# Optimization experiments

Measured on AMD Instinct MI355X. Metric: run time of the kernel, lower is better.

## Reference

```python
import jax, jax.numpy as jnp
import numpy as np

B, L, C, K = 8, 4096, 256, 3
PAD = 1  # (K-1)//2, required so offset/mask conv preserves length L


def conv1d(x, w, b, padding):
    # x: (B, C, L), w: (O, C, K), b: (O,)
    y = jax.lax.conv_general_dilated(
        x, w, window_strides=(1,), padding=[(padding, padding)],
        dimension_numbers=('NCH', 'OIH', 'NCH'))
    return y + b[None, :, None]


def setup_inputs() -> dict:
    key = jax.random.key(0)
    ks = jax.random.split(key, 5)
    fan = 1.0 / np.sqrt(C * K)
    return {
        'x': jax.random.normal(ks[0], (B, L, C), dtype=jnp.float32),
        'w_off': jax.random.uniform(ks[1], (K, C, K), jnp.float32, -fan, fan),
        'b_off': jax.random.uniform(ks[2], (K,), jnp.float32, -fan, fan),
        'w_mask': jax.random.uniform(ks[3], (K, C, K), jnp.float32, -fan, fan),
        'b_mask': jax.random.uniform(ks[4], (K,), jnp.float32, -fan, fan),
    }


def reference(x, w_off, b_off, w_mask, b_mask):
    b, l, c = x.shape
    xt = jnp.transpose(x, (0, 2, 1))                      # (B, C, L)
    offset = conv1d(xt, w_off, b_off, PAD)                # (B, K, L)
    mask = jax.nn.sigmoid(conv1d(xt, w_mask, b_mask, PAD))  # (B, K, L)

    # pos = l + offset, clamped; offset is shared across channels.
    i = jnp.arange(l, dtype=x.dtype)[None, None, :]       # (1, 1, L)
    pos = jnp.clip(i + offset, 0.0, l - 1)                # (B, K, L)
    fl = jnp.floor(pos).astype(jnp.int32)                 # (B, K, L)
    ce = jnp.minimum(fl + 1, l - 1)
    alpha = pos - fl.astype(x.dtype)                      # (B, K, L)

    # gather per batch: (C, L)[:, (K, L)] -> (C, K, L)
    gather = jax.vmap(lambda xb, idx: xb[:, idx])
    x_floor = gather(xt, fl)                              # (B, C, K, L)
    x_ceil = gather(xt, ce)                               # (B, C, K, L)
    a = alpha[:, None, :, :]
    sampled = x_floor * (1.0 - a) + x_ceil * a            # (B, C, K, L)

    out = (sampled * mask[:, None, :, :]).sum(axis=2)     # (B, C, L)
    # Faithful to torch: output.view(B, L, out_channels) is a raw reshape
    # of the contiguous (B, C, L) buffer, NOT a transpose.
    return out.reshape(b, l, c)
```

## Files before the change

kernel.cpp:

```cpp
#include <hip/hip_runtime.h>
#include <math.h>

#define B_  8
#define L_  4096
#define C_  256
#define TL  32
#define NT  2

template<int CTRL, int RM>
__device__ __forceinline__ float dpp_add(float v) {
    int mv = __builtin_amdgcn_update_dpp(0, __float_as_int(v), CTRL, RM, 0xf, true);
    return v + __int_as_float(mv);
}
__device__ __forceinline__ float wave_sum_hi(float v) {
    v = dpp_add<0xB1, 0xf>(v);
    v = dpp_add<0x4E, 0xf>(v);
    v = dpp_add<0x141, 0xf>(v);
    v = dpp_add<0x140, 0xf>(v);
    v = dpp_add<0x142, 0xa>(v);
    v = dpp_add<0x143, 0xc>(v);
    return v;
}
__device__ __forceinline__ float bcast63(float v) {
    return __int_as_float(__builtin_amdgcn_readlane(__float_as_int(v), 63));
}

__global__ __launch_bounds__(512, 4)
void dconv1d_kernel(const float* __restrict__ x,
                    const float* __restrict__ w_off,
                    const float* __restrict__ b_off,
                    const float* __restrict__ w_mask,
                    const float* __restrict__ b_mask,
                    float* __restrict__ out) {
    __shared__ float s_tile[TL * C_];

    const int tid  = threadIdx.x;
    const int lane = tid & 63;
    const int wv   = tid >> 6;
    const int b    = blockIdx.y;
    const float* __restrict__ xb = x + (size_t)b * L_ * C_;

    const float bo0 = b_off[0],  bo1 = b_off[1],  bo2 = b_off[2];
    const float bm0 = b_mask[0], bm1 = b_mask[1], bm2 = b_mask[2];

    const int c4 = lane << 2;

    for (int t = 0; t < NT; ++t) {
        const int l0  = (blockIdx.x * NT + t) * TL;
        const int lb4 = l0 + wv * 4;

        float4 xrow[6];
        #pragma unroll
        for (int rr = 0; rr < 6; ++rr) {
            const int row = lb4 - 1 + rr;
            if (row >= 0 && row < L_)
                xrow[rr] = *reinterpret_cast<const float4*>(
                    xb + (size_t)row * C_ + c4);
            else
                xrow[rr] = make_float4(0.f, 0.f, 0.f, 0.f);
        }

        float sums[4][6];
        #pragma unroll
        for (int o = 0; o < 6; ++o) {
            const float* ws = (o < 3) ? (w_off + o * (C_ * 3))
                                      : (w_mask + (o - 3) * (C_ * 3));
            const float4* wp = reinterpret_cast<const float4*>(ws + lane * 12);
            const float4 w0 = wp[0], w1 = wp[1], w2 = wp[2];
            float acc[4] = {0.f, 0.f, 0.f, 0.f};
            #pragma unroll
            for (int rr = 0; rr < 6; ++rr) {
                #pragma unroll
                for (int tt = 0; tt < 3; ++tt) {
                    const int i = rr - tt;
                    if (i >= 0 && i < 4) {
                        const float wt0 = (tt==0)?w0.x:((tt==1)?w0.y:w0.z);
                        const float wt1 = (tt==0)?w0.w:((tt==1)?w1.x:w1.y);
                        const float wt2 = (tt==0)?w1.z:((tt==1)?w1.w:w2.x);
                        const float wt3 = (tt==0)?w2.y:((tt==1)?w2.z:w2.w);
                        acc[i] += xrow[rr].x * wt0 + xrow[rr].y * wt1
                                + xrow[rr].z * wt2 + xrow[rr].w * wt3;
                    }
                }
            }
            #pragma unroll
            for (int i = 0; i < 4; ++i)
                sums[i][o] = bcast63(wave_sum_hi(acc[i]));
        }

        #pragma unroll
        for (int i = 0; i < 4; ++i) {
            const int ll = wv * 4 + i;
            const int l  = l0 + ll;
            float4 v = make_float4(0.f, 0.f, 0.f, 0.f);
            #pragma unroll
            for (int k = 0; k < 3; ++k) {
                const float bo = (k == 0) ? bo0 : ((k == 1) ? bo1 : bo2);
                const float bm = (k == 0) ? bm0 : ((k == 1) ? bm1 : bm2);
                const float off = sums[i][k] + bo;
                const float pos = fminf(fmaxf((float)l + off, 0.0f), (float)(L_ - 1));
                const float flf = floorf(pos);
                const int   fl  = (int)flf;
                const int   ce  = min(fl + 1, L_ - 1);
                const float a   = pos - flf;
                const float m   = 1.0f / (1.0f + __expf(-(sums[i][k + 3] + bm)));
                const float wf  = m * (1.0f - a);
                const float wc  = m * a;
                const float4 xf = *reinterpret_cast<const float4*>(
                    xb + (size_t)fl * C_ + c4);
                const float4 xc = *reinterpret_cast<const float4*>(
                    xb + (size_t)ce * C_ + c4);
                v.x += wf * xf.x + wc * xc.x;
                v.y += wf * xf.y + wc * xc.y;
                v.z += wf * xf.z + wc * xc.z;
                v.w += wf * xf.w + wc * xc.w;
            }
            const int gr = lane ^ (ll & 15);
            *reinterpret_cast<float4*>(&s_tile[ll * C_ + (gr << 2)]) = v;
        }
        __syncthreads();

        {
            const int lw = tid & 31;
            const int q0 = tid >> 5;
            #pragma unroll
            for (int s = 0; s < 4; ++s) {
                const int q  = q0 + (s << 4);
                const int gr = q ^ (lw & 15);
                const float4 v = *reinterpret_cast<const float4*>(
                    &s_tile[lw * C_ + (gr << 2)]);
                const size_t ob = ((size_t)b * C_ + (q << 2)) * L_ + l0 + lw;
                out[ob]          = v.x;
                out[ob + L_]     = v.y;
                out[ob + 2 * L_] = v.z;
                out[ob + 3 * L_] = v.w;
            }
        }
        __syncthreads();
    }
}

extern "C" void kernel_launch(void* const* d_in, const int* in_sizes, int n_in,
                              void* d_out, int out_size, void* d_ws, size_t ws_size,
                              hipStream_t stream) {
    const float* x      = (const float*)d_in[0];
    const float* w_off  = (const float*)d_in[1];
    const float* b_off  = (const float*)d_in[2];
    const float* w_mask = (const float*)d_in[3];
    const float* b_mask = (const float*)d_in[4];
    float* out = (float*)d_out;

    dim3 grid(L_ / (TL * NT), B_);
    dconv1d_kernel<<<grid, 512, 0, stream>>>(x, w_off, b_off, w_mask, b_mask, out);
}
```

Measured before the change: 28.25 us.

## Stage x tile with halo in LDS and serve gathers from shared memory

Each block now loads a 40-row halo tile of x into LDS once. The conv reads and the deformable gather reads are served from LDS when the sampled positions fall within the tile, with a fallback to global memory otherwise. The block shrinks to 256 threads, each wave handles 8 positions, the NT loop goes away, and the grid doubles in x. The new layout uses more LDS per block (about 72KB), which lowers occupancy, and the tile must fill completely before any compute can start.

```diff
diff --git a/kernel.cpp b/kernel.cpp
--- a/kernel.cpp
+++ b/kernel.cpp
@@ -5,7 +5,8 @@
 #define L_  4096
 #define C_  256
 #define TL  32
-#define NT  2
+#define SROWS 40
+#define SBASE 4
 
 template<int CTRL, int RM>
 __device__ __forceinline__ float dpp_add(float v) {
@@ -25,18 +26,22 @@
     return __int_as_float(__builtin_amdgcn_readlane(__float_as_int(v), 63));
 }
 
-__global__ __launch_bounds__(512, 4)
+#define LDS_BARRIER() asm volatile("s_waitcnt lgkmcnt(0)\ns_barrier" ::: "memory")
+
+__global__ __launch_bounds__(256, 2)
 void dconv1d_kernel(const float* __restrict__ x,
                     const float* __restrict__ w_off,
                     const float* __restrict__ b_off,
                     const float* __restrict__ w_mask,
                     const float* __restrict__ b_mask,
                     float* __restrict__ out) {
+    __shared__ float s_x[SROWS * C_];
     __shared__ float s_tile[TL * C_];
 
     const int tid  = threadIdx.x;
     const int lane = tid & 63;
     const int wv   = tid >> 6;
+    const int l0   = blockIdx.x * TL;
     const int b    = blockIdx.y;
     const float* __restrict__ xb = x + (size_t)b * L_ * C_;
 
@@ -45,98 +50,104 @@
 
     const int c4 = lane << 2;
 
-    for (int t = 0; t < NT; ++t) {
-        const int l0  = (blockIdx.x * NT + t) * TL;
-        const int lb4 = l0 + wv * 4;
+    #pragma unroll
+    for (int j = 0; j < (SROWS * 64) / 256; ++j) {
+        const int idx  = j * 256 + tid;
+        const int r    = idx >> 6;
+        const int gq   = idx & 63;
+        const int grow = l0 - SBASE + r;
+        float4 v = make_float4(0.f, 0.f, 0.f, 0.f);
+        if (grow >= 0 && grow < L_)
+            v = *reinterpret_cast<const float4*>(xb + (size_t)grow * C_ + (gq << 2));
+        *reinterpret_cast<float4*>(&s_x[r * C_ + (gq << 2)]) = v;
+    }
+    LDS_BARRIER();
 
-        float4 xrow[6];
+    const int lw0 = wv * 8;
+    float sums[8][6];
+    #pragma unroll
+    for (int o = 0; o < 6; ++o) {
+        const float* ws = (o < 3) ? (w_off + o * (C_ * 3))
+                                  : (w_mask + (o - 3) * (C_ * 3));
+        const float4* wp = reinterpret_cast<const float4*>(ws + lane * 12);
+        const float4 w0 = wp[0], w1 = wp[1], w2 = wp[2];
+        float acc[8] = {0.f,0.f,0.f,0.f,0.f,0.f,0.f,0.f};
         #pragma unroll
-        for (int rr = 0; rr < 6; ++rr) {
-            const int row = lb4 - 1 + rr;
-            if (row >= 0 && row < L_)
-                xrow[rr] = *reinterpret_cast<const float4*>(
-                    xb + (size_t)row * C_ + c4);
-            else
-                xrow[rr] = make_float4(0.f, 0.f, 0.f, 0.f);
-        }
-
-        float sums[4][6];
-        #pragma unroll
-        for (int o = 0; o < 6; ++o) {
-            const float* ws = (o < 3) ? (w_off + o * (C_ * 3))
-                                      : (w_mask + (o - 3) * (C_ * 3));
-            const float4* wp = reinterpret_cast<const float4*>(ws + lane * 12);
-            const float4 w0 = wp[0], w1 = wp[1], w2 = wp[2];
-            float acc[4] = {0.f, 0.f, 0.f, 0.f};
+        for (int rr = 0; rr < 10; ++rr) {
+            const int srow = lw0 - 1 + rr + SBASE;
+            const float4 xv = *reinterpret_cast<const float4*>(
+                &s_x[srow * C_ + c4]);
             #pragma unroll
-            for (int rr = 0; rr < 6; ++rr) {
-                #pragma unroll
-                for (int tt = 0; tt < 3; ++tt) {
-                    const int i = rr - tt;
-                    if (i >= 0 && i < 4) {
-                        const float wt0 = (tt==0)?w0.x:((tt==1)?w0.y:w0.z);
-                        const float wt1 = (tt==0)?w0.w:((tt==1)?w1.x:w1.y);
-                        const float wt2 = (tt==0)?w1.z:((tt==1)?w1.w:w2.x);
-                        const float wt3 = (tt==0)?w2.y:((tt==1)?w2.z:w2.w);
-                        acc[i] += xrow[rr].x * wt0 + xrow[rr].y * wt1
-                                + xrow[rr].z * wt2 + xrow[rr].w * wt3;
-                    }
+            for (int tt = 0; tt < 3; ++tt) {
+                const int i = rr - tt;
+                if (i >= 0 && i < 8) {
+                    const float wt0 = (tt==0)?w0.x:((tt==1)?w0.y:w0.z);
+                    const float wt1 = (tt==0)?w0.w:((tt==1)?w1.x:w1.y);
+                    const float wt2 = (tt==0)?w1.z:((tt==1)?w1.w:w2.x);
+                    const float wt3 = (tt==0)?w2.y:((tt==1)?w2.z:w2.w);
+                    acc[i] += xv.x * wt0 + xv.y * wt1
+                            + xv.z * wt2 + xv.w * wt3;
                 }
             }
-            #pragma unroll
-            for (int i = 0; i < 4; ++i)
-                sums[i][o] = bcast63(wave_sum_hi(acc[i]));
         }
+        #pragma unroll
+        for (int i = 0; i < 8; ++i)
+            sums[i][o] = bcast63(wave_sum_hi(acc[i]));
+    }
 
+    #pragma unroll
+    for (int i = 0; i < 8; ++i) {
+        const int ll = lw0 + i;
+        const int l  = l0 + ll;
+        float4 v = make_float4(0.f, 0.f, 0.f, 0.f);
         #pragma unroll
-        for (int i = 0; i < 4; ++i) {
-            const int ll = wv * 4 + i;
-            const int l  = l0 + ll;
-            float4 v = make_float4(0.f, 0.f, 0.f, 0.f);
-            #pragma unroll
-            for (int k = 0; k < 3; ++k) {
-                const float bo = (k == 0) ? bo0 : ((k == 1) ? bo1 : bo2);
-                const float bm = (k == 0) ? bm0 : ((k == 1) ? bm1 : bm2);
-                const float off = sums[i][k] + bo;
-                const float pos = fminf(fmaxf((float)l + off, 0.0f), (float)(L_ - 1));
-                const float flf = floorf(pos);
-                const int   fl  = (int)flf;
-                const int   ce  = min(fl + 1, L_ - 1);
-                const float a   = pos - flf;
-                const float m   = 1.0f / (1.0f + __expf(-(sums[i][k + 3] + bm)));
-                const float wf  = m * (1.0f - a);
-                const float wc  = m * a;
-                const float4 xf = *reinterpret_cast<const float4*>(
-                    xb + (size_t)fl * C_ + c4);
-                const float4 xc = *reinterpret_cast<const float4*>(
-                    xb + (size_t)ce * C_ + c4);
-                v.x += wf * xf.x + wc * xc.x;
-                v.y += wf * xf.y + wc * xc.y;
-                v.z += wf * xf.z + wc * xc.z;
-                v.w += wf * xf.w + wc * xc.w;
+        for (int k = 0; k < 3; ++k) {
+            const float bo = (k == 0) ? bo0 : ((k == 1) ? bo1 : bo2);
+            const float bm = (k == 0) ? bm0 : ((k == 1) ? bm1 : bm2);
+            const float off = sums[i][k] + bo;
+            const float pos = fminf(fmaxf((float)l + off, 0.0f), (float)(L_ - 1));
+            const float flf = floorf(pos);
+            const int   fl  = (int)flf;
+            const int   ce  = min(fl + 1, L_ - 1);
+            const float a   = pos - flf;
+            const float m   = 1.0f / (1.0f + __expf(-(sums[i][k + 3] + bm)));
+            const float wf  = m * (1.0f - a);
+            const float wc  = m * a;
+            const int fr = fl - (l0 - SBASE);
+            const int cr = ce - (l0 - SBASE);
+            float4 xf, xc;
+            if (fr >= 0 && cr < SROWS) {
+                xf = *reinterpret_cast<const float4*>(&s_x[fr * C_ + c4]);
+                xc = *reinterpret_cast<const float4*>(&s_x[cr * C_ + c4]);
+            } else {
+                xf = *reinterpret_cast<const float4*>(xb + (size_t)fl * C_ + c4);
+                xc = *reinterpret_cast<const float4*>(xb + (size_t)ce * C_ + c4);
             }
-            const int gr = lane ^ (ll & 15);
-            *reinterpret_cast<float4*>(&s_tile[ll * C_ + (gr << 2)]) = v;
+            v.x += wf * xf.x + wc * xc.x;
+            v.y += wf * xf.y + wc * xc.y;
+            v.z += wf * xf.z + wc * xc.z;
+            v.w += wf * xf.w + wc * xc.w;
         }
-        __syncthreads();
+        const int gr = lane ^ (ll & 15);
+        *reinterpret_cast<float4*>(&s_tile[ll * C_ + (gr << 2)]) = v;
+    }
+    LDS_BARRIER();
 
-        {
-            const int lw = tid & 31;
-            const int q0 = tid >> 5;
-            #pragma unroll
-            for (int s = 0; s < 4; ++s) {
-                const int q  = q0 + (s << 4);
-                const int gr = q ^ (lw & 15);
-                const float4 v = *reinterpret_cast<const float4*>(
-                    &s_tile[lw * C_ + (gr << 2)]);
-                const size_t ob = ((size_t)b * C_ + (q << 2)) * L_ + l0 + lw;
-                out[ob]          = v.x;
-                out[ob + L_]     = v.y;
-                out[ob + 2 * L_] = v.z;
-                out[ob + 3 * L_] = v.w;
-            }
+    {
+        const int lw = tid & 31;
+        const int q0 = tid >> 5;
+        #pragma unroll
+        for (int s = 0; s < 8; ++s) {
+            const int q  = q0 + (s << 3);
+            const int gr = q ^ (lw & 15);
+            const float4 v = *reinterpret_cast<const float4*>(
+                &s_tile[lw * C_ + (gr << 2)]);
+            const size_t ob = ((size_t)b * C_ + (q << 2)) * L_ + l0 + lw;
+            out[ob]          = v.x;
+            out[ob + L_]     = v.y;
+            out[ob + 2 * L_] = v.z;
+            out[ob + 3 * L_] = v.w;
         }
-        __syncthreads();
     }
 }
 
@@ -150,6 +161,6 @@
     const float* b_mask = (const float*)d_in[4];
     float* out = (float*)d_out;
 
-    dim3 grid(L_ / (TL * NT), B_);
-    dconv1d_kernel<<<grid, 512, 0, stream>>>(x, w_off, b_off, w_mask, b_mask, out);
+    dim3 grid(L_ / TL, B_);
+    dconv1d_kernel<<<grid, 256, 0, stream>>>(x, w_off, b_off, w_mask, b_mask, out);
 }
```

New measurement: 34.01 us. 1.2x slower.
